# Performance work log

Measured on AMD Instinct MI355X. Metric: run time of the kernel, lower is better.

Reference implementation:

```python
import jax, jax.numpy as jnp
import numpy as np

FS = 2  # dilated kernel size
DILS = tuple(2 ** i for _ in range(2) for i in range(10))  # 2 blocks x 10 layers
LWS = tuple((FS - 1) * d for d in DILS)  # left-wing shrink of each dilated conv
TOTAL_LW = sum(LWS)  # 2046


def _conv(x, w, dil=1):
    # x: (B, Cin, T), w: (Cout, Cin, K), valid causal (left-wing) conv
    return jax.lax.conv_general_dilated(x, w, (1,), 'VALID', rhs_dilation=(dil,),
                                        dimension_numbers=('NCH', 'OIH', 'NCH'))


def _tconv(x, w, stride):
    # PyTorch ConvTranspose1d(n,n,k,stride,padding=k-stride): out_len = S*stride + stride - k
    wf = jnp.flip(w, -1).transpose(1, 0, 2)  # (in,out,k) -> (out,in,k), flipped taps
    return jax.lax.conv_general_dilated(x, wf, (1,), [(stride - 1, stride - 1)],
                                        lhs_dilation=(stride,),
                                        dimension_numbers=('NCH', 'OIH', 'NCH'))


def _wavenet(wav, lc_sparse, lc_conv_w, lc_conv_b, ups_w0, ups_b0, ups_w1, ups_b1,
             ups_w2, ups_b2, ups_w3, ups_b3, emb_w, emb_b, base_w, base_b,
             sig_w, sig_b, gate_w, gate_b, psig_w, pgate_w, skp_w, res_w,
             post1_w, post1_b, post2_w, post2_b, speaker_inds, jitter_index):
    # jitter local conditioning frames along time
    lc = jnp.take_along_axis(lc_sparse, jitter_index[:, None, :], axis=2)
    # post-jitter conv (kernel 3, valid)
    lc = _conv(lc, lc_conv_w) + lc_conv_b[:, None]
    # upsampling chain to audio rate
    for w, b, s in ((ups_w0, ups_b0, 5), (ups_w1, ups_b1, 4), (ups_w2, ups_b2, 4), (ups_w3, ups_b3, 4)):
        lc = _tconv(lc, w, s) + b[:, None]
    # global (speaker) conditioning: Linear applied to one-hot == column gather
    gc = emb_w[:, speaker_inds].T + emb_b  # (B, G)
    cond = jnp.concatenate(
        [lc, jnp.broadcast_to(gc[:, :, None], gc.shape + (lc.shape[2],))], axis=1)  # (B, I+G, T0)
    # base 1x1 conv onto residual channels; wav already trimmed to T0 = cond length
    x = _conv(wav, base_w) + base_b[:, None]
    skp_sum = jnp.zeros(())
    cum = 0
    for i, (dil, lw) in enumerate(zip(DILS, LWS)):
        cl = cum + lw                      # cond lead aligning cond to this layer's output
        c = cond[:, :, cl:]
        filt = _conv(x, sig_w[i], dil) + sig_b[i][:, None] + _conv(c, psig_w[i])
        gate = _conv(x, gate_w[i], dil) + gate_b[i][:, None] + _conv(c, pgate_w[i])
        z = jnp.tanh(filt) * jax.nn.sigmoid(gate)
        sl = TOTAL_LW - cl                 # skip lead aligning z to final output length
        skp_sum = skp_sum + _conv(z[:, :, sl:], skp_w[i])
        x = _conv(z, res_w[i]) + x[:, :, lw:]
        cum = cl
    h = jax.nn.relu(skp_sum)
    h = jax.nn.relu(_conv(h, post1_w) + post1_b[:, None])
    h = _conv(h, post2_w) + post2_b[:, None]
    return jax.nn.log_softmax(h, axis=1)  # (B, n_quant, T_final)


def setup_inputs() -> dict:
    key = jax.random.key(0)
    ks = iter(jax.random.split(key, 64))
    B, S = 4, 64
    NLC_IN, NLC_OUT, NSPK, NGE = 64, 128, 40, 128
    NQ, NR, ND, NS, NP = 256, 384, 256, 256, 512
    NCOND = NLC_OUT + NGE
    L = 20
    T = 18308  # (((64-2)*5+5-25)*4+4-16)... upsampled cond length == wav length

    def rn(shape, scale=0.05):
        return jax.random.normal(next(ks), shape, jnp.float32) * scale

    return dict(
        wav=rn((B, NQ, T), 1.0),
        lc_sparse=rn((B, NLC_IN, S), 1.0),
        lc_conv_w=rn((NLC_OUT, NLC_IN, 3)), lc_conv_b=rn((NLC_OUT,)),
        ups_w0=rn((NLC_OUT, NLC_OUT, 25)), ups_b0=rn((NLC_OUT,)),
        ups_w1=rn((NLC_OUT, NLC_OUT, 16)), ups_b1=rn((NLC_OUT,)),
        ups_w2=rn((NLC_OUT, NLC_OUT, 16)), ups_b2=rn((NLC_OUT,)),
        ups_w3=rn((NLC_OUT, NLC_OUT, 16)), ups_b3=rn((NLC_OUT,)),
        emb_w=rn((NGE, NSPK)), emb_b=rn((NGE,)),
        base_w=rn((NR, NQ, 1)), base_b=rn((NR,)),
        sig_w=rn((L, ND, NR, FS)), sig_b=rn((L, ND)),
        gate_w=rn((L, ND, NR, FS)), gate_b=rn((L, ND)),
        psig_w=rn((L, ND, NCOND, 1)), pgate_w=rn((L, ND, NCOND, 1)),
        skp_w=rn((L, NS, ND, 1)), res_w=rn((L, NR, ND, 1)),
        post1_w=rn((NP, NS, 1)), post1_b=rn((NP,)),
        post2_w=rn((NQ, NP, 1)), post2_b=rn((NQ,)),
        speaker_inds=jax.random.randint(next(ks), (B,), 0, NSPK),
        jitter_index=jax.random.randint(next(ks), (B, S), 0, S),
    )


def reference(wav, lc_sparse, lc_conv_w, lc_conv_b, ups_w0, ups_b0, ups_w1, ups_b1,
              ups_w2, ups_b2, ups_w3, ups_b3, emb_w, emb_b, base_w, base_b,
              sig_w, sig_b, gate_w, gate_b, psig_w, pgate_w, skp_w, res_w,
              post1_w, post1_b, post2_w, post2_b, speaker_inds, jitter_index):
    return _wavenet(wav, lc_sparse, lc_conv_w, lc_conv_b, ups_w0, ups_b0, ups_w1, ups_b1,
                    ups_w2, ups_b2, ups_w3, ups_b3, emb_w, emb_b, base_w, base_b,
                    sig_w, sig_b, gate_w, gate_b, psig_w, pgate_w, skp_w, res_w,
                    post1_w, post1_b, post2_w, post2_b, speaker_inds, jitter_index)
```

## Files before the change

kernel.cpp:

```cpp
#include <hip/hip_runtime.h>
#include <hip/hip_bf16.h>
#include <math.h>


#define T_IN 18308
#define T_OUT 16262

typedef unsigned short u16;
typedef unsigned int u32;
typedef __attribute__((ext_vector_type(8))) short short8_t;
typedef __attribute__((ext_vector_type(4))) float f32x4;

__device__ __forceinline__ float bf2f(u16 h) { return __uint_as_float(((u32)h) << 16); }
__device__ __forceinline__ u16 f2bf(float f) {
  u32 u = __float_as_uint(f);
  return (u16)((u + 0x7fffu + ((u >> 16) & 1u)) >> 16);
}

__global__ void k_pack_frag(const float* __restrict__ src, u16* __restrict__ dst,
                            int M, int K, int L, long src_lstride) {
  int nks = K >> 5;
  long per = (long)M * K;
  long total = per * L;
  for (long idx = blockIdx.x * (long)blockDim.x + threadIdx.x; idx < total; idx += (long)gridDim.x * blockDim.x) {
    int l = (int)(idx / per); long r = idx - (long)l * per;
    int j = (int)(r & 7); int lane = (int)((r >> 3) & 63); int fid = (int)(r >> 9);
    int ks = fid % nks; int mt = fid / nks;
    int row = mt * 16 + (lane & 15);
    int col = ks * 32 + ((lane >> 4) << 3) + j;
    dst[idx] = f2bf(src[l * src_lstride + (long)row * K + col]);
  }
}

__global__ void k_pack_frag_gau(const float* __restrict__ sig_w, const float* __restrict__ gate_w,
                                const float* __restrict__ psig_w, const float* __restrict__ pgate_w,
                                u16* __restrict__ dstF, u16* __restrict__ dstG) {
  const long per = 229376;
  long total = per * 20;
  for (long idx = blockIdx.x * (long)blockDim.x + threadIdx.x; idx < total; idx += (long)gridDim.x * blockDim.x) {
    int l = (int)(idx / per); long r = idx - (long)l * per;
    int j = (int)(r & 7); int lane = (int)((r >> 3) & 63); int fid = (int)(r >> 9);
    int ks = fid % 28; int mt = fid / 28;
    int row = mt * 16 + (lane & 15);
    int k = ks * 32 + ((lane >> 4) << 3) + j;
    float vF, vG;
    if (k < 384) {
      vF = sig_w[(((long)l * 256 + row) * 384 + k) * 2 + 0];
      vG = gate_w[(((long)l * 256 + row) * 384 + k) * 2 + 0];
    } else if (k < 768) {
      vF = sig_w[(((long)l * 256 + row) * 384 + (k - 384)) * 2 + 1];
      vG = gate_w[(((long)l * 256 + row) * 384 + (k - 384)) * 2 + 1];
    } else {
      vF = psig_w[((long)l * 256 + row) * 256 + (k - 768)];
      vG = pgate_w[((long)l * 256 + row) * 256 + (k - 768)];
    }
    dstF[idx] = f2bf(vF);
    dstG[idx] = f2bf(vG);
  }
}
// ... 123 lines not shown
    }
    __syncthreads();
  }
  #pragma unroll
  for (int jj = 0; jj < 4; ++jj) {
    int j = j0 + tn * 4 + jj;
    int t = j * S + p;
    if (t >= Lout) continue;
    #pragma unroll
    for (int i = 0; i < 4; ++i) {
      int o = bm0 + tm * 4 + i;
      yout[((long)b * 128 + o) * ostride + t] = acc[i][jj] + bias[o];
    }
  }
}

__global__ __launch_bounds__(256) void k_tconv4m(
    const u16* __restrict__ im, const u16* __restrict__ Wp4,
    const float* __restrict__ bias, u16* __restrict__ out) {
  int lane = threadIdx.x & 63, wave = threadIdx.x >> 6;
  int b = blockIdx.z;
  int p = blockIdx.y >> 1, chb = (blockIdx.y & 1) << 6;
  int tbase = (blockIdx.x << 8) + (wave << 6);
  int lrow = lane & 15, lk = (lane >> 4) << 3;
  int mt0 = chb >> 4;
  const u16* Wp = Wp4 + (long)p * 65536;
  f32x4 zed = {0.f, 0.f, 0.f, 0.f};
  f32x4 acc[4][4];
  #pragma unroll
  for (int m = 0; m < 4; ++m)
    #pragma unroll
    for (int n = 0; n < 4; ++n) acc[m][n] = zed;
  const u16* ib = im + (long)b * 4580 * 512;
  for (int ks = 0; ks < 16; ++ks) {
    short8_t a[4];
    #pragma unroll
    for (int m = 0; m < 4; ++m)
      a[m] = *(const short8_t*)(Wp + ((long)((mt0 + m) * 16 + ks) << 9) + (lane << 3));
    #pragma unroll
    for (int n = 0; n < 4; ++n) {
      int j = tbase + (n << 4) + lrow;
      j = min(j, 4579);
      short8_t bv = *(const short8_t*)(ib + (long)j * 512 + (ks << 5) + lk);
      #pragma unroll
      for (int m = 0; m < 4; ++m)
        acc[m][n] = __builtin_amdgcn_mfma_f32_16x16x32_bf16(a[m], bv, acc[m][n], 0, 0, 0);
    }
  }
  #pragma unroll
  for (int n = 0; n < 4; ++n) {
    int j = tbase + (n << 4) + lrow;
    int t = j * 4 + p;
    if (t >= T_IN) continue;
    #pragma unroll
    for (int m = 0; m < 4; ++m) {
      int ch0 = chb + (m << 4) + ((lane >> 4) << 2);
      f32x4 bb = *(const f32x4*)(bias + ch0);
      ushort4 o;
      o.x = f2bf(acc[m][n][0] + bb[0]);
      o.y = f2bf(acc[m][n][1] + bb[1]);
      o.z = f2bf(acc[m][n][2] + bb[2]);
      o.w = f2bf(acc[m][n][3] + bb[3]);
      *(ushort4*)(out + ((long)b * T_IN + t) * 128 + ch0) = o;
    }
  }
}

__global__ __launch_bounds__(256) void k_wav_t(const float* __restrict__ wav, u16* __restrict__ dst) {
  __shared__ float xs[32][65];
  int b = blockIdx.z, c0 = blockIdx.y * 32, t0 = blockIdx.x * 64;
  int tid = threadIdx.x;
  #pragma unroll
  for (int i = 0; i < 8; ++i) {
    int idx = tid + i * 256;
    int c = idx >> 6, tl = idx & 63;
    int t = t0 + tl; if (t >= T_IN) t = T_IN - 1;
    xs[c][tl] = wav[((long)b * 256 + c0 + c) * T_IN + t];
  }
  __syncthreads();
  #pragma unroll
  for (int i = 0; i < 8; ++i) {
    int idx = tid + i * 256;
    int tl = idx >> 5, c = idx & 31;
    int t = t0 + tl;
    if (t < T_IN) dst[((long)b * T_IN + t) * 256 + c0 + c] = f2bf(xs[c][tl]);
  }
}

__global__ __launch_bounds__(256) void k_basem(
    const u16* __restrict__ wavT, const u16* __restrict__ Wp,
    const float* __restrict__ bias, u16* __restrict__ X) {
  int lane = threadIdx.x & 63, wave = threadIdx.x >> 6;
  int b = blockIdx.z, chb = blockIdx.y << 6;
  int tbase = (blockIdx.x << 8) + (wave << 6);
  int lrow = lane & 15, lk = (lane >> 4) << 3;
  int mt0 = chb >> 4;
  f32x4 zed = {0.f, 0.f, 0.f, 0.f};
  f32x4 acc[4][4];
  #pragma unroll
  for (int m = 0; m < 4; ++m)
    #pragma unroll
    for (int n = 0; n < 4; ++n) acc[m][n] = zed;
  const u16* xb = wavT + (long)b * T_IN * 256;
  for (int ks = 0; ks < 8; ++ks) {
    short8_t a[4];
    #pragma unroll
    for (int m = 0; m < 4; ++m)
      a[m] = *(const short8_t*)(Wp + ((long)((mt0 + m) * 8 + ks) << 9) + (lane << 3));
    #pragma unroll
    for (int n = 0; n < 4; ++n) {
      int row = tbase + (n << 4) + lrow;
      row = min(row, T_IN - 1);
      short8_t bv = *(const short8_t*)(xb + (long)row * 256 + (ks << 5) + lk);
      #pragma unroll
      for (int m = 0; m < 4; ++m)
        acc[m][n] = __builtin_amdgcn_mfma_f32_16x16x32_bf16(a[m], bv, acc[m][n], 0, 0, 0);
    }
  }
  #pragma unroll
  for (int n = 0; n < 4; ++n) {
    int t = tbase + (n << 4) + lrow;
    if (t >= T_IN) continue;
    #pragma unroll
    for (int m = 0; m < 4; ++m) {
      int ch0 = chb + (m << 4) + ((lane >> 4) << 2);
      f32x4 bb = *(const f32x4*)(bias + ch0);
      ushort4 o;
      o.x = f2bf(acc[m][n][0] + bb[0]);
      o.y = f2bf(acc[m][n][1] + bb[1]);
      o.z = f2bf(acc[m][n][2] + bb[2]);
      o.w = f2bf(acc[m][n][3] + bb[3]);
      *(ushort4*)(X + ((long)b * T_IN + t) * 384 + ch0) = o;
    }
  }
}

__global__ __launch_bounds__(256, 3) void k_gau6(
    const u16* __restrict__ Xc, const u16* __restrict__ Lc,
    const u16* __restrict__ WpF, const u16* __restrict__ WpG,
    const float* __restrict__ cb, u16* __restrict__ Z,
    int Lz, int d, int cl, int nt) {
  __shared__ __align__(16) u16 stg[2][8192];
  int lane = threadIdx.x & 63, wave = threadIdx.x >> 6;
  int bx = blockIdx.x;
  int tb = ((bx >> 4) << 3) + (bx & 7);
  int chh = (bx >> 3) & 1;
  if (tb >= nt) return;
  int tbase = tb << 6;
  int b = blockIdx.z;
  int chb = (chh << 7) + (wave << 5);
  int mt0 = chb >> 4;
  int lrow = lane & 15, lk16 = lane >> 4;
  const u16* xb = Xc + (long)b * T_IN * 384;
  const u16* lb = Lc + (long)b * T_IN * 128;
  const u16* pWF0 = WpF + (((long)mt0 * 28) << 9) + (lane << 3);
  const u16* pWF1 = WpF + (((long)(mt0 + 1) * 28) << 9) + (lane << 3);
  const u16* pWG0 = WpG + (((long)mt0 * 28) << 9) + (lane << 3);
  const u16* pWG1 = WpG + (((long)(mt0 + 1) * 28) << 9) + (lane << 3);
  int r0 = tbase + (wave << 4) + lrow;
  const u16* s0 = xb + (long)min(r0, T_IN - 1) * 384 + (lk16 << 3);
  const u16* s1 = xb + (long)min(r0 + d, T_IN - 1) * 384 + (lk16 << 3);
  const u16* s2 = lb + (long)min(r0 + cl, T_IN - 1) * 128 + (lk16 << 3);
  u16* wd = &stg[0][0] + (wave << 9) + (lane << 3);

  f32x4 zed = {0.f, 0.f, 0.f, 0.f};
  f32x4 accF[2][4], accG[2][4];
  #pragma unroll
  for (int m = 0; m < 2; ++m)
    #pragma unroll
    for (int n = 0; n < 4; ++n) { accF[m][n] = zed; accG[m][n] = zed; }

  #pragma unroll
  for (int j = 0; j < 4; ++j)
    *(short8_t*)(wd + (j << 11)) = *(const short8_t*)(s0 + (j << 5));
  __syncthreads();

  #pragma unroll
  for (int ss = 0; ss < 7; ++ss) {
    short8_t nv0, nv1, nv2, nv3;
    if (ss < 6) {
      int kb = ss * 4 + 4;
      const u16* p0 = (kb + 0 < 12) ? (s0 + ((kb + 0) << 5)) : (kb + 0 < 24) ? (s1 + ((kb - 12) << 5)) : (s2 + ((kb - 24) << 5));
      const u16* p1 = (kb + 1 < 12) ? (s0 + ((kb + 1) << 5)) : (kb + 1 < 24) ? (s1 + ((kb - 11) << 5)) : (s2 + ((kb - 23) << 5));
      const u16* p2 = (kb + 2 < 12) ? (s0 + ((kb + 2) << 5)) : (kb + 2 < 24) ? (s1 + ((kb - 10) << 5)) : (s2 + ((kb - 22) << 5));
      const u16* p3 = (kb + 3 < 12) ? (s0 + ((kb + 3) << 5)) : (kb + 3 < 24) ? (s1 + ((kb - 9) << 5)) : (s2 + ((kb - 21) << 5));
      nv0 = *(const short8_t*)p0;
      nv1 = *(const short8_t*)p1;
      nv2 = *(const short8_t*)p2;
      nv3 = *(const short8_t*)p3;
    }
    const u16* bufc = &stg[ss & 1][0];
    #pragma unroll
    for (int j = 0; j < 4; ++j) {
      int ks = ss * 4 + j;
      short8_t af0 = *(const short8_t*)(pWF0 + (ks << 9));
      short8_t af1 = *(const short8_t*)(pWF1 + (ks << 9));
      short8_t ag0 = *(const short8_t*)(pWG0 + (ks << 9));
      short8_t ag1 = *(const short8_t*)(pWG1 + (ks << 9));
      #pragma unroll
      for (int n = 0; n < 4; ++n) {
        short8_t bv = *(const short8_t*)(bufc + (j << 11) + (n << 9) + (lane << 3));
        accF[0][n] = __builtin_amdgcn_mfma_f32_16x16x32_bf16(af0, bv, accF[0][n], 0, 0, 0);
        accF[1][n] = __builtin_amdgcn_mfma_f32_16x16x32_bf16(af1, bv, accF[1][n], 0, 0, 0);
        accG[0][n] = __builtin_amdgcn_mfma_f32_16x16x32_bf16(ag0, bv, accG[0][n], 0, 0, 0);
        accG[1][n] = __builtin_amdgcn_mfma_f32_16x16x32_bf16(ag1, bv, accG[1][n], 0, 0, 0);
      }
    }
    if (ss < 6) {
      u16* wdn = wd + (((ss + 1) & 1) << 13);
      *(short8_t*)(wdn + (0 << 11)) = nv0;
      *(short8_t*)(wdn + (1 << 11)) = nv1;
      *(short8_t*)(wdn + (2 << 11)) = nv2;
      *(short8_t*)(wdn + (3 << 11)) = nv3;
    }
    __syncthreads();
  }

  const float* cbF = cb + b * 256;
  const float* cbG = cb + 1024 + b * 256;
  #pragma unroll
  for (int n = 0; n < 4; ++n) {
    int t = tbase + (n << 4) + lrow;
    if (t >= Lz) continue;
    #pragma unroll
    for (int m = 0; m < 2; ++m) {
      int ch0 = chb + (m << 4) + (lk16 << 2);
      f32x4 bf = *(const f32x4*)(cbF + ch0);
      f32x4 bg = *(const f32x4*)(cbG + ch0);
      ushort4 o;
      #pragma unroll
      for (int r = 0; r < 4; ++r) {
        float f = accF[m][n][r] + bf[r];
        float g = accG[m][n][r] + bg[r];
        f = fminf(fmaxf(f, -15.f), 15.f);
        float e2 = __expf(2.f * f);
        float th = 1.f - 2.f * __builtin_amdgcn_rcpf(e2 + 1.f);
        float sg = __builtin_amdgcn_rcpf(1.f + __expf(-g));
        u16 zz = f2bf(th * sg);
        if (r == 0) o.x = zz; else if (r == 1) o.y = zz; else if (r == 2) o.z = zz; else o.w = zz;
      }
      *(ushort4*)(Z + ((long)b * T_IN + t) * 256 + ch0) = o;
    }
  }
}

__global__ __launch_bounds__(256, 3) void k_skipres6(
    const u16* __restrict__ Zb, const u16* __restrict__ Wskp, const u16* __restrict__ Wres,
    const u16* __restrict__ Xres, float* __restrict__ skip, u16* __restrict__ Xout,
    int Lz, int sl, int lw, int first) {
  __shared__ __align__(16) u16 stg[16384];
  int lane = threadIdx.x & 63, wave = threadIdx.x >> 6;
  int slice = blockIdx.x;
  int tbase = blockIdx.y << 6;
  int b = blockIdx.z;
  bool issk = slice < 2;
  int mt0 = (issk ? slice * 8 : (slice - 2) * 8) + (wave << 1);
  const u16* Wp = issk ? Wskp : Wres;
  int lrow = lane & 15, lk16 = lane >> 4;
  const u16* pW0 = Wp + (((long)mt0 * 8) << 9) + (lane << 3);
  const u16* pW1 = Wp + (((long)(mt0 + 1) * 8) << 9) + (lane << 3);
  const u16* zb = Zb + (long)b * T_IN * 256;
  int r0 = min(tbase + (wave << 4) + lrow, T_IN - 1);
  const u16* sz = zb + (long)r0 * 256 + (lk16 << 3);
  u16* wd = &stg[0] + (wave << 9) + (lane << 3);
  f32x4 zed = {0.f, 0.f, 0.f, 0.f};
  f32x4 acc[2][4];
  #pragma unroll
  for (int m = 0; m < 2; ++m)
    #pragma unroll
    for (int n = 0; n < 4; ++n) acc[m][n] = zed;

  #pragma unroll
  for (int j = 0; j < 8; ++j)
    *(short8_t*)(wd + (j << 11)) = *(const short8_t*)(sz + (j << 5));
  __syncthreads();

  #pragma unroll
  for (int ks = 0; ks < 8; ++ks) {
    short8_t a0 = *(const short8_t*)(pW0 + (ks << 9));
    short8_t a1 = *(const short8_t*)(pW1 + (ks << 9));
    #pragma unroll
    for (int n = 0; n < 4; ++n) {
      short8_t bv = *(const short8_t*)(&stg[0] + (ks << 11) + (n << 9) + (lane << 3));
      acc[0][n] = __builtin_amdgcn_mfma_f32_16x16x32_bf16(a0, bv, acc[0][n], 0, 0, 0);
      acc[1][n] = __builtin_amdgcn_mfma_f32_16x16x32_bf16(a1, bv, acc[1][n], 0, 0, 0);
    }
  }
  #pragma unroll
  for (int n = 0; n < 4; ++n) {
    int tg = tbase + (n << 4) + lrow;
    #pragma unroll
    for (int m = 0; m < 2; ++m) {
      int ch0 = ((mt0 + m) << 4) + (lk16 << 2);
      if (issk) {
        if (tg >= sl && tg < Lz) {
          float* p = skip + ((long)b * T_OUT + (tg - sl)) * 256 + ch0;
          if (first) { *(f32x4*)p = acc[m][n]; }
          else { f32x4 v = *(f32x4*)p; v += acc[m][n]; *(f32x4*)p = v; }
        }
      } else if (tg < Lz) {
        const u16* rp = Xres + ((long)b * T_IN + tg + lw) * 384 + ch0;
        ushort4 rv = *(const ushort4*)rp;
        ushort4 o;
        o.x = f2bf(acc[m][n][0] + bf2f(rv.x));
        o.y = f2bf(acc[m][n][1] + bf2f(rv.y));
        o.z = f2bf(acc[m][n][2] + bf2f(rv.z));
        o.w = f2bf(acc[m][n][3] + bf2f(rv.w));
        *(ushort4*)(Xout + ((long)b * T_IN + tg) * 384 + ch0) = o;
      }
    }
  }
}

__global__ __launch_bounds__(256) void k_post1(
    const float* __restrict__ skip, const u16* __restrict__ Wp,
    const float* __restrict__ b1, u16* __restrict__ h1) {
  int lane = threadIdx.x & 63, wave = threadIdx.x >> 6;
  int b = blockIdx.z, qb = blockIdx.y << 6;
  int tbase = (blockIdx.x << 8) + (wave << 6);
  int lrow = lane & 15, lk = (lane >> 4) << 3;
  int mt0 = qb >> 4;
  f32x4 zed = {0.f, 0.f, 0.f, 0.f};
  f32x4 acc[4][4];
  #pragma unroll
  for (int m = 0; m < 4; ++m)
    #pragma unroll
    for (int n = 0; n < 4; ++n) acc[m][n] = zed;
  const float* sb = skip + (long)b * T_OUT * 256;
  for (int ks = 0; ks < 8; ++ks) {
    short8_t a[4];
    #pragma unroll
    for (int m = 0; m < 4; ++m)
      a[m] = *(const short8_t*)(Wp + ((long)((mt0 + m) * 8 + ks) << 9) + (lane << 3));
    #pragma unroll
    for (int n = 0; n < 4; ++n) {
      int row = tbase + (n << 4) + lrow;
      row = min(row, T_OUT - 1);
      const float* src = sb + (long)row * 256 + (ks << 5) + lk;
      f32x4 v0 = *(const f32x4*)src;
      f32x4 v1 = *(const f32x4*)(src + 4);
      short8_t bv;
      #pragma unroll
      for (int j = 0; j < 4; ++j) bv[j] = (short)f2bf(fmaxf(v0[j], 0.f));
      #pragma unroll
      for (int j = 0; j < 4; ++j) bv[4 + j] = (short)f2bf(fmaxf(v1[j], 0.f));
      #pragma unroll
      for (int m = 0; m < 4; ++m)
        acc[m][n] = __builtin_amdgcn_mfma_f32_16x16x32_bf16(a[m], bv, acc[m][n], 0, 0, 0);
    }
  }
  #pragma unroll
  for (int n = 0; n < 4; ++n) {
    int t = tbase + (n << 4) + lrow;
    if (t >= T_OUT) continue;
    #pragma unroll
    for (int m = 0; m < 4; ++m) {
      int ch0 = qb + (m << 4) + ((lane >> 4) << 2);
      f32x4 bb = *(const f32x4*)(b1 + ch0);
      ushort4 o;
      o.x = f2bf(fmaxf(acc[m][n][0] + bb[0], 0.f));
      o.y = f2bf(fmaxf(acc[m][n][1] + bb[1], 0.f));
      o.z = f2bf(fmaxf(acc[m][n][2] + bb[2], 0.f));
      o.w = f2bf(fmaxf(acc[m][n][3] + bb[3], 0.f));
// ... 91 lines not shown
    }
  }
}

extern "C" void kernel_launch(void* const* d_in, const int* in_sizes, int n_in,
                              void* d_out, int out_size, void* d_ws, size_t ws_size,
                              hipStream_t stream) {
  const float* wav       = (const float*)d_in[0];
  const float* lc_sparse = (const float*)d_in[1];
  const float* lc_conv_w = (const float*)d_in[2];
  const float* lc_conv_b = (const float*)d_in[3];
  const float* ups_w[4]  = {(const float*)d_in[4], (const float*)d_in[6], (const float*)d_in[8], (const float*)d_in[10]};
  const float* ups_b[4]  = {(const float*)d_in[5], (const float*)d_in[7], (const float*)d_in[9], (const float*)d_in[11]};
  const float* emb_w     = (const float*)d_in[12];
  const float* emb_b     = (const float*)d_in[13];
  const float* base_w    = (const float*)d_in[14];
  const float* base_b    = (const float*)d_in[15];
  const float* sig_w     = (const float*)d_in[16];
  const float* sig_b     = (const float*)d_in[17];
  const float* gate_w    = (const float*)d_in[18];
  const float* gate_b    = (const float*)d_in[19];
  const float* psig_w    = (const float*)d_in[20];
  const float* pgate_w   = (const float*)d_in[21];
  const float* skp_w     = (const float*)d_in[22];
  const float* res_w     = (const float*)d_in[23];
  const float* post1_w   = (const float*)d_in[24];
  const float* post1_b   = (const float*)d_in[25];
  const float* post2_w   = (const float*)d_in[26];
  const float* post2_b   = (const float*)d_in[27];
  const int* spk         = (const int*)d_in[28];
  const int* jit         = (const int*)d_in[29];
  float* out = (float*)d_out;

  size_t off = 0;
  auto alloc = [&](size_t bytes) -> void* {
    off = (off + 255) & ~(size_t)255;
    void* p = (char*)d_ws + off;
    off += bytes;
    return p;
  };
  u16* wfgF   = (u16*)alloc(20L * 229376 * 2);
  u16* wfgG   = (u16*)alloc(20L * 229376 * 2);
  u16* wskpF  = (u16*)alloc(20L * 65536 * 2);
  u16* wresF  = (u16*)alloc(20L * 98304 * 2);
  u16* wbaseF = (u16*)alloc(384L * 256 * 2);
  u16* wp1F   = (u16*)alloc(512L * 256 * 2);
  u16* wp2F   = (u16*)alloc(256L * 512 * 2);
  float* wtc1 = (float*)alloc(5L * 640 * 128 * 4);
  float* wtc2 = (float*)alloc(4L * 512 * 128 * 4);
  float* wtc3 = (float*)alloc(4L * 512 * 128 * 4);
  u16* wtc4F  = (u16*)alloc(4L * 65536 * 2);
  float* cbias = (float*)alloc(20L * 2 * 4 * 256 * 4);
  float* gc    = (float*)alloc(4L * 128 * 4);
  u16* lcbf    = (u16*)alloc(4L * T_IN * 128 * 2);
  u16* xA      = (u16*)alloc(4L * T_IN * 384 * 2);
  u16* xB      = (u16*)alloc(4L * T_IN * 384 * 2);
  u16* zbuf    = (u16*)alloc(4L * T_IN * 256 * 2);
  float* skip  = (float*)alloc(4L * T_OUT * 256 * 4);
  float* lcs0 = (float*)zbuf;
  float* lcs1 = lcs0 + 4L * 128 * 64;
  float* lcs2 = lcs1 + 4L * 128 * 290;
  float* lcs3 = lcs2 + 4L * 128 * 1148;
  u16* im3    = xB;
  u16* wavT   = (u16*)skip;
  u16* h1bf   = xA;
  (void)ws_size; (void)in_sizes; (void)n_in; (void)out_size;

  k_pack_frag_gau<<<4480, 256, 0, stream>>>(sig_w, gate_w, psig_w, pgate_w, wfgF, wfgG);
  k_pack_frag<<<1280, 256, 0, stream>>>(skp_w, wskpF, 256, 256, 20, 256L * 256);
  k_pack_frag<<<1920, 256, 0, stream>>>(res_w, wresF, 384, 256, 20, 384L * 256);
  k_pack_frag<<<96, 256, 0, stream>>>(base_w, wbaseF, 384, 256, 1, 0);
  k_pack_frag<<<128, 256, 0, stream>>>(post1_w, wp1F, 512, 256, 1, 0);
  k_pack_frag<<<128, 256, 0, stream>>>(post2_w, wp2F, 256, 512, 1, 0);
  k_pack_tconv<<<320, 256, 0, stream>>>(ups_w[0], wtc1, 5, 25, 5);
  k_pack_tconv<<<256, 256, 0, stream>>>(ups_w[1], wtc2, 4, 16, 4);
  k_pack_tconv<<<256, 256, 0, stream>>>(ups_w[2], wtc3, 4, 16, 4);
  k_pack_tc4f<<<256, 256, 0, stream>>>(ups_w[3], wtc4F);
  k_gc<<<1, 512, 0, stream>>>(emb_w, emb_b, spk, gc);
  k_cbias<<<dim3(20, 8), 256, 0, stream>>>(psig_w, pgate_w, sig_b, gate_b, gc, cbias);

  k_lc0<<<dim3(4, 62), 128, 0, stream>>>(lc_sparse, jit, lc_conv_w, lc_conv_b, lcs0);
  k_tconvg<5><<<dim3(1, 10, 4), 256, 0, stream>>>(lcs0, 62, 64, lcs1, 290, 290, wtc1, ups_b[0], 5);
  k_tconvg<4><<<dim3(5, 8, 4), 256, 0, stream>>>(lcs1, 290, 290, lcs2, 1148, 1148, wtc2, ups_b[1], 4);
  k_tconvg<4><<<dim3(18, 8, 4), 256, 0, stream>>>(lcs2, 1148, 1148, lcs3, 4580, 4580, wtc3, ups_b[2], 4);
  k_im2col3<<<2048, 256, 0, stream>>>(lcs3, im3);
  k_tconv4m<<<dim3(18, 8, 4), 256, 0, stream>>>(im3, wtc4F, ups_b[3], lcbf);

  k_wav_t<<<dim3(287, 8, 4), 256, 0, stream>>>(wav, wavT);
  k_basem<<<dim3(72, 6, 4), 256, 0, stream>>>(wavT, wbaseF, base_b, xA);

  static const int DILS[20] = {1, 2, 4, 8, 16, 32, 64, 128, 256, 512,
                               1, 2, 4, 8, 16, 32, 64, 128, 256, 512};
  int cum = 0;
  u16* xc = xA; u16* xn = xB;
  for (int l = 0; l < 20; ++l) {
    int dd = DILS[l], lw = dd, cl = cum + lw;
    int Lz = T_IN - cl;
    int sl = 2046 - cl;
    int nt = (Lz + 63) / 64;
    int gx = 16 * ((nt + 7) >> 3);
    k_gau6<<<dim3(gx, 1, 4), 256, 0, stream>>>(
        xc, lcbf, wfgF + (long)l * 229376, wfgG + (long)l * 229376,
        cbias + (long)l * 2048, zbuf, Lz, dd, cl, nt);
    int nsl = (l == 19) ? 2 : 5;
    k_skipres6<<<dim3(nsl, nt, 4), 256, 0, stream>>>(
        zbuf, wskpF + (long)l * 65536, wresF + (long)l * 98304,
        xc, skip, xn, Lz, sl, lw, (l == 0) ? 1 : 0);
    cum = cl;
    u16* t = xc; xc = xn; xn = t;
  }

  k_post1<<<dim3(64, 8, 4), 256, 0, stream>>>(skip, wp1F, post1_b, h1bf);
  k_post2sm<<<dim3(255, 1, 4), 256, 0, stream>>>(h1bf, wp2F, post2_b, out);
}
```

Baseline: 3.617 ms.

## Store activations in MFMA fragment-tiled layout and load B operands directly

After: 4.530 ms. +25.2%, slower.

```diff
diff --git a/kernel.cpp b/kernel.cpp
--- a/kernel.cpp
+++ b/kernel.cpp
@@ -5,6 +5,10 @@
 
 #define T_IN 18308
 #define T_OUT 16262
+#define NT16 1152
+#define XTB (1152L * 12 * 512)
+#define ZTB (1152L * 8 * 512)
+#define LTB (1152L * 4 * 512)
 
 typedef unsigned short u16;
 typedef unsigned int u32;
@@ -234,6 +238,7 @@
     int j = tbase + (n << 4) + lrow;
     int t = j * 4 + p;
     if (t >= T_IN) continue;
+    int tt16 = t >> 4, tr = t & 15;
     #pragma unroll
     for (int m = 0; m < 4; ++m) {
       int ch0 = chb + (m << 4) + ((lane >> 4) << 2);
@@ -243,7 +248,8 @@
       o.y = f2bf(acc[m][n][1] + bb[1]);
       o.z = f2bf(acc[m][n][2] + bb[2]);
       o.w = f2bf(acc[m][n][3] + bb[3]);
-      *(ushort4*)(out + ((long)b * T_IN + t) * 128 + ch0) = o;
+      long addr = ((long)tt16 * 4 + (ch0 >> 5)) * 512 + ((ch0 & 31) >> 3) * 128 + tr * 8 + (ch0 & 7);
+      *(ushort4*)(out + (long)b * LTB + addr) = o;
     }
   }
 }
@@ -303,6 +309,7 @@
   for (int n = 0; n < 4; ++n) {
     int t = tbase + (n << 4) + lrow;
     if (t >= T_IN) continue;
+    int t16 = (tbase >> 4) + n;
     #pragma unroll
     for (int m = 0; m < 4; ++m) {
       int ch0 = chb + (m << 4) + ((lane >> 4) << 2);
@@ -312,39 +319,43 @@
       o.y = f2bf(acc[m][n][1] + bb[1]);
       o.z = f2bf(acc[m][n][2] + bb[2]);
       o.w = f2bf(acc[m][n][3] + bb[3]);
-      *(ushort4*)(X + ((long)b * T_IN + t) * 384 + ch0) = o;
-    }
-  }
-}
-
-__global__ __launch_bounds__(256, 3) void k_gau6(
+      long addr = ((long)t16 * 12 + (ch0 >> 5)) * 512 + ((ch0 & 31) >> 3) * 128 + lrow * 8 + (ch0 & 7);
+      *(ushort4*)(X + (long)b * XTB + addr) = o;
+    }
+  }
+}
+
+__global__ __launch_bounds__(256, 4) void k_gau7(
     const u16* __restrict__ Xc, const u16* __restrict__ Lc,
     const u16* __restrict__ WpF, const u16* __restrict__ WpG,
     const float* __restrict__ cb, u16* __restrict__ Z,
     int Lz, int d, int cl, int nt) {
-  __shared__ __align__(16) u16 stg[2][8192];
   int lane = threadIdx.x & 63, wave = threadIdx.x >> 6;
   int bx = blockIdx.x;
   int tb = ((bx >> 4) << 3) + (bx & 7);
   int chh = (bx >> 3) & 1;
   if (tb >= nt) return;
-  int tbase = tb << 6;
+  int tbase = tb << 6, tb4 = tb << 2;
   int b = blockIdx.z;
   int chb = (chh << 7) + (wave << 5);
   int mt0 = chb >> 4;
-  int lrow = lane & 15, lk16 = lane >> 4;
-  const u16* xb = Xc + (long)b * T_IN * 384;
-  const u16* lb = Lc + (long)b * T_IN * 128;
+  int lrow = lane & 15, loct = lane >> 4;
+  const u16* xb = Xc + (long)b * XTB;
+  const u16* lb = Lc + (long)b * LTB;
   const u16* pWF0 = WpF + (((long)mt0 * 28) << 9) + (lane << 3);
   const u16* pWF1 = WpF + (((long)(mt0 + 1) * 28) << 9) + (lane << 3);
   const u16* pWG0 = WpG + (((long)mt0 * 28) << 9) + (lane << 3);
   const u16* pWG1 = WpG + (((long)(mt0 + 1) * 28) << 9) + (lane << 3);
-  int r0 = tbase + (wave << 4) + lrow;
-  const u16* s0 = xb + (long)min(r0, T_IN - 1) * 384 + (lk16 << 3);
-  const u16* s1 = xb + (long)min(r0 + d, T_IN - 1) * 384 + (lk16 << 3);
-  const u16* s2 = lb + (long)min(r0 + cl, T_IN - 1) * 128 + (lk16 << 3);
-  u16* wd = &stg[0][0] + (wave << 9) + (lane << 3);
-
+  int P0[4], P1[4], P2[4];
+  #pragma unroll
+  for (int n = 0; n < 4; ++n) {
+    int T0 = tbase + (n << 4) + lrow;
+    P0[n] = (T0 >> 4) * 6144 + loct * 128 + (T0 & 15) * 8;
+    int T1 = T0 + d;
+    P1[n] = (T1 >> 4) * 6144 + loct * 128 + (T1 & 15) * 8;
+    int T2 = T0 + cl;
+    P2[n] = (T2 >> 4) * 2048 + loct * 128 + (T2 & 15) * 8;
+  }
   f32x4 zed = {0.f, 0.f, 0.f, 0.f};
   f32x4 accF[2][4], accG[2][4];
   #pragma unroll
@@ -353,49 +364,22 @@
     for (int n = 0; n < 4; ++n) { accF[m][n] = zed; accG[m][n] = zed; }
 
   #pragma unroll
-  for (int j = 0; j < 4; ++j)
-    *(short8_t*)(wd + (j << 11)) = *(const short8_t*)(s0 + (j << 5));
-  __syncthreads();
-
-  #pragma unroll
-  for (int ss = 0; ss < 7; ++ss) {
-    short8_t nv0, nv1, nv2, nv3;
-    if (ss < 6) {
-      int kb = ss * 4 + 4;
-      const u16* p0 = (kb + 0 < 12) ? (s0 + ((kb + 0) << 5)) : (kb + 0 < 24) ? (s1 + ((kb - 12) << 5)) : (s2 + ((kb - 24) << 5));
-      const u16* p1 = (kb + 1 < 12) ? (s0 + ((kb + 1) << 5)) : (kb + 1 < 24) ? (s1 + ((kb - 11) << 5)) : (s2 + ((kb - 23) << 5));
-      const u16* p2 = (kb + 2 < 12) ? (s0 + ((kb + 2) << 5)) : (kb + 2 < 24) ? (s1 + ((kb - 10) << 5)) : (s2 + ((kb - 22) << 5));
-      const u16* p3 = (kb + 3 < 12) ? (s0 + ((kb + 3) << 5)) : (kb + 3 < 24) ? (s1 + ((kb - 9) << 5)) : (s2 + ((kb - 21) << 5));
-      nv0 = *(const short8_t*)p0;
-      nv1 = *(const short8_t*)p1;
-      nv2 = *(const short8_t*)p2;
-      nv3 = *(const short8_t*)p3;
-    }
-    const u16* bufc = &stg[ss & 1][0];
-    #pragma unroll
-    for (int j = 0; j < 4; ++j) {
-      int ks = ss * 4 + j;
-      short8_t af0 = *(const short8_t*)(pWF0 + (ks << 9));
-      short8_t af1 = *(const short8_t*)(pWF1 + (ks << 9));
-      short8_t ag0 = *(const short8_t*)(pWG0 + (ks << 9));
-      short8_t ag1 = *(const short8_t*)(pWG1 + (ks << 9));
-      #pragma unroll
-      for (int n = 0; n < 4; ++n) {
-        short8_t bv = *(const short8_t*)(bufc + (j << 11) + (n << 9) + (lane << 3));
-        accF[0][n] = __builtin_amdgcn_mfma_f32_16x16x32_bf16(af0, bv, accF[0][n], 0, 0, 0);
-        accF[1][n] = __builtin_amdgcn_mfma_f32_16x16x32_bf16(af1, bv, accF[1][n], 0, 0, 0);
-        accG[0][n] = __builtin_amdgcn_mfma_f32_16x16x32_bf16(ag0, bv, accG[0][n], 0, 0, 0);
-        accG[1][n] = __builtin_amdgcn_mfma_f32_16x16x32_bf16(ag1, bv, accG[1][n], 0, 0, 0);
-      }
-    }
-    if (ss < 6) {
-      u16* wdn = wd + (((ss + 1) & 1) << 13);
-      *(short8_t*)(wdn + (0 << 11)) = nv0;
-      *(short8_t*)(wdn + (1 << 11)) = nv1;
-      *(short8_t*)(wdn + (2 << 11)) = nv2;
-      *(short8_t*)(wdn + (3 << 11)) = nv3;
-    }
-    __syncthreads();
+  for (int ks = 0; ks < 28; ++ks) {
+    short8_t af0 = *(const short8_t*)(pWF0 + (ks << 9));
+    short8_t af1 = *(const short8_t*)(pWF1 + (ks << 9));
+    short8_t ag0 = *(const short8_t*)(pWG0 + (ks << 9));
+    short8_t ag1 = *(const short8_t*)(pWG1 + (ks << 9));
+    #pragma unroll
+    for (int n = 0; n < 4; ++n) {
+      const u16* src = (ks < 12) ? (xb + P0[n] + (ks << 9))
+                     : (ks < 24) ? (xb + P1[n] + ((ks - 12) << 9))
+                                 : (lb + P2[n] + ((ks - 24) << 9));
+      short8_t bv = *(const short8_t*)src;
+      accF[0][n] = __builtin_amdgcn_mfma_f32_16x16x32_bf16(af0, bv, accF[0][n], 0, 0, 0);
+      accF[1][n] = __builtin_amdgcn_mfma_f32_16x16x32_bf16(af1, bv, accF[1][n], 0, 0, 0);
+      accG[0][n] = __builtin_amdgcn_mfma_f32_16x16x32_bf16(ag0, bv, accG[0][n], 0, 0, 0);
+      accG[1][n] = __builtin_amdgcn_mfma_f32_16x16x32_bf16(ag1, bv, accG[1][n], 0, 0, 0);
+    }
   }
 
   const float* cbF = cb + b * 256;
@@ -406,7 +390,7 @@
     if (t >= Lz) continue;
     #pragma unroll
     for (int m = 0; m < 2; ++m) {
-      int ch0 = chb + (m << 4) + (lk16 << 2);
+      int ch0 = chb + (m << 4) + (loct << 2);
       f32x4 bf = *(const f32x4*)(cbF + ch0);
       f32x4 bg = *(const f32x4*)(cbG + ch0);
       ushort4 o;
@@ -421,41 +405,36 @@
         u16 zz = f2bf(th * sg);
         if (r == 0) o.x = zz; else if (r == 1) o.y = zz; else if (r == 2) o.z = zz; else o.w = zz;
       }
-      *(ushort4*)(Z + ((long)b * T_IN + t) * 256 + ch0) = o;
-    }
-  }
-}
-
-__global__ __launch_bounds__(256, 3) void k_skipres6(
-    const u16* __restrict__ Zb, const u16* __restrict__ Wskp, const u16* __restrict__ Wres,
+      long addr = ((long)(tb4 + n) * 8 + (ch0 >> 5)) * 512 + ((ch0 & 31) >> 3) * 128 + lrow * 8 + (ch0 & 7);
+      *(ushort4*)(Z + (long)b * ZTB + addr) = o;
+    }
+  }
+}
+
+__global__ __launch_bounds__(256, 4) void k_skipres7(
+    const u16* __restrict__ Zt, const u16* __restrict__ Wskp, const u16* __restrict__ Wres,
     const u16* __restrict__ Xres, float* __restrict__ skip, u16* __restrict__ Xout,
     int Lz, int sl, int lw, int first) {
-  __shared__ __align__(16) u16 stg[16384];
   int lane = threadIdx.x & 63, wave = threadIdx.x >> 6;
   int slice = blockIdx.x;
-  int tbase = blockIdx.y << 6;
+  int tbase = blockIdx.y << 6, tb4 = blockIdx.y << 2;
   int b = blockIdx.z;
   bool issk = slice < 2;
   int mt0 = (issk ? slice * 8 : (slice - 2) * 8) + (wave << 1);
   const u16* Wp = issk ? Wskp : Wres;
-  int lrow = lane & 15, lk16 = lane >> 4;
+  int lrow = lane & 15, loct = lane >> 4;
   const u16* pW0 = Wp + (((long)mt0 * 8) << 9) + (lane << 3);
   const u16* pW1 = Wp + (((long)(mt0 + 1) * 8) << 9) + (lane << 3);
-  const u16* zb = Zb + (long)b * T_IN * 256;
-  int r0 = min(tbase + (wave << 4) + lrow, T_IN - 1);
-  const u16* sz = zb + (long)r0 * 256 + (lk16 << 3);
-  u16* wd = &stg[0] + (wave << 9) + (lane << 3);
+  const u16* zb = Zt + (long)b * ZTB;
+  int Pz[4];
+  #pragma unroll
+  for (int n = 0; n < 4; ++n) Pz[n] = ((tb4 + n) * 8) * 512 + lane * 8;
   f32x4 zed = {0.f, 0.f, 0.f, 0.f};
   f32x4 acc[2][4];
   #pragma unroll
   for (int m = 0; m < 2; ++m)
     #pragma unroll
     for (int n = 0; n < 4; ++n) acc[m][n] = zed;
-
-  #pragma unroll
-  for (int j = 0; j < 8; ++j)
-    *(short8_t*)(wd + (j << 11)) = *(const short8_t*)(sz + (j << 5));
-  __syncthreads();
 
   #pragma unroll
   for (int ks = 0; ks < 8; ++ks) {
@@ -463,7 +442,7 @@
     short8_t a1 = *(const short8_t*)(pW1 + (ks << 9));
     #pragma unroll
     for (int n = 0; n < 4; ++n) {
-      short8_t bv = *(const short8_t*)(&stg[0] + (ks << 11) + (n << 9) + (lane << 3));
+      short8_t bv = *(const short8_t*)(zb + Pz[n] + (ks << 9));
       acc[0][n] = __builtin_amdgcn_mfma_f32_16x16x32_bf16(a0, bv, acc[0][n], 0, 0, 0);
       acc[1][n] = __builtin_amdgcn_mfma_f32_16x16x32_bf16(a1, bv, acc[1][n], 0, 0, 0);
     }
@@ -473,7 +452,7 @@
     int tg = tbase + (n << 4) + lrow;
     #pragma unroll
     for (int m = 0; m < 2; ++m) {
-      int ch0 = ((mt0 + m) << 4) + (lk16 << 2);
+      int ch0 = ((mt0 + m) << 4) + (loct << 2);
       if (issk) {
         if (tg >= sl && tg < Lz) {
           float* p = skip + ((long)b * T_OUT + (tg - sl)) * 256 + ch0;
@@ -481,14 +460,16 @@
           else { f32x4 v = *(f32x4*)p; v += acc[m][n]; *(f32x4*)p = v; }
         }
       } else if (tg < Lz) {
-        const u16* rp = Xres + ((long)b * T_IN + tg + lw) * 384 + ch0;
-        ushort4 rv = *(const ushort4*)rp;
+        int T = tg + lw;
+        long ra = ((long)(T >> 4) * 12 + (ch0 >> 5)) * 512 + ((ch0 & 31) >> 3) * 128 + (T & 15) * 8 + (ch0 & 7);
+        ushort4 rv = *(const ushort4*)(Xres + (long)b * XTB + ra);
         ushort4 o;
         o.x = f2bf(acc[m][n][0] + bf2f(rv.x));
         o.y = f2bf(acc[m][n][1] + bf2f(rv.y));
         o.z = f2bf(acc[m][n][2] + bf2f(rv.z));
         o.w = f2bf(acc[m][n][3] + bf2f(rv.w));
-        *(ushort4*)(Xout + ((long)b * T_IN + tg) * 384 + ch0) = o;
+        long wa = ((long)(tb4 + n) * 12 + (ch0 >> 5)) * 512 + ((ch0 & 31) >> 3) * 128 + lrow * 8 + (ch0 & 7);
+        *(ushort4*)(Xout + (long)b * XTB + wa) = o;
       }
     }
   }
@@ -688,10 +669,10 @@
   u16* wtc4F  = (u16*)alloc(4L * 65536 * 2);
   float* cbias = (float*)alloc(20L * 2 * 4 * 256 * 4);
   float* gc    = (float*)alloc(4L * 128 * 4);
-  u16* lcbf    = (u16*)alloc(4L * T_IN * 128 * 2);
-  u16* xA      = (u16*)alloc(4L * T_IN * 384 * 2);
-  u16* xB      = (u16*)alloc(4L * T_IN * 384 * 2);
-  u16* zbuf    = (u16*)alloc(4L * T_IN * 256 * 2);
+  u16* lcbf    = (u16*)alloc(4L * LTB * 2);
+  u16* xA      = (u16*)alloc(4L * XTB * 2);
+  u16* xB      = (u16*)alloc(4L * XTB * 2);
+  u16* zbuf    = (u16*)alloc(4L * ZTB * 2);
   float* skip  = (float*)alloc(4L * T_OUT * 256 * 4);
   float* lcs0 = (float*)zbuf;
   float* lcs1 = lcs0 + 4L * 128 * 64;
@@ -735,11 +716,11 @@
     int sl = 2046 - cl;
     int nt = (Lz + 63) / 64;
     int gx = 16 * ((nt + 7) >> 3);
-    k_gau6<<<dim3(gx, 1, 4), 256, 0, stream>>>(
+    k_gau7<<<dim3(gx, 1, 4), 256, 0, stream>>>(
         xc, lcbf, wfgF + (long)l * 229376, wfgG + (long)l * 229376,
         cbias + (long)l * 2048, zbuf, Lz, dd, cl, nt);
     int nsl = (l == 19) ? 2 : 5;
-    k_skipres6<<<dim3(nsl, nt, 4), 256, 0, stream>>>(
+    k_skipres7<<<dim3(nsl, nt, 4), 256, 0, stream>>>(
         zbuf, wskpF + (long)l * 65536, wresF + (long)l * 98304,
         xc, skip, xn, Lz, sl, lw, (l == 0) ? 1 : 0);
     cum = cl;
```

## Split filter and gate GEMMs across waves with 128-step time tiles in gated unit

Applied to the files above, without the earlier changes.

Measured after the change: 3.686 ms. About the same (+1.9%).

```diff
diff --git a/kernel.cpp b/kernel.cpp
--- a/kernel.cpp
+++ b/kernel.cpp
@@ -317,28 +317,28 @@
   }
 }
 
-__global__ __launch_bounds__(256, 3) void k_gau6(
+__global__ __launch_bounds__(512, 4) void k_gau8(
     const u16* __restrict__ Xc, const u16* __restrict__ Lc,
     const u16* __restrict__ WpF, const u16* __restrict__ WpG,
     const float* __restrict__ cb, u16* __restrict__ Z,
     int Lz, int d, int cl, int nt) {
-  __shared__ __align__(16) u16 stg[2][8192];
+  __shared__ __align__(16) u16 stg[2][16384];
   int lane = threadIdx.x & 63, wave = threadIdx.x >> 6;
   int bx = blockIdx.x;
   int tb = ((bx >> 4) << 3) + (bx & 7);
   int chh = (bx >> 3) & 1;
   if (tb >= nt) return;
-  int tbase = tb << 6;
+  int tbase = tb << 7;
   int b = blockIdx.z;
-  int chb = (chh << 7) + (wave << 5);
+  int fg = wave & 1, chq = wave >> 1;
+  int chb = (chh << 7) + (chq << 5);
   int mt0 = chb >> 4;
   int lrow = lane & 15, lk16 = lane >> 4;
   const u16* xb = Xc + (long)b * T_IN * 384;
   const u16* lb = Lc + (long)b * T_IN * 128;
-  const u16* pWF0 = WpF + (((long)mt0 * 28) << 9) + (lane << 3);
-  const u16* pWF1 = WpF + (((long)(mt0 + 1) * 28) << 9) + (lane << 3);
-  const u16* pWG0 = WpG + (((long)mt0 * 28) << 9) + (lane << 3);
-  const u16* pWG1 = WpG + (((long)(mt0 + 1) * 28) << 9) + (lane << 3);
+  const u16* Wsel = fg ? WpG : WpF;
+  const u16* pW0 = Wsel + (((long)mt0 * 28) << 9) + (lane << 3);
+  const u16* pW1 = Wsel + (((long)(mt0 + 1) * 28) << 9) + (lane << 3);
   int r0 = tbase + (wave << 4) + lrow;
   const u16* s0 = xb + (long)min(r0, T_IN - 1) * 384 + (lk16 << 3);
   const u16* s1 = xb + (long)min(r0 + d, T_IN - 1) * 384 + (lk16 << 3);
@@ -346,18 +346,17 @@
   u16* wd = &stg[0][0] + (wave << 9) + (lane << 3);
 
   f32x4 zed = {0.f, 0.f, 0.f, 0.f};
-  f32x4 accF[2][4], accG[2][4];
+  f32x4 acc[2][8];
   #pragma unroll
   for (int m = 0; m < 2; ++m)
     #pragma unroll
-    for (int n = 0; n < 4; ++n) { accF[m][n] = zed; accG[m][n] = zed; }
+    for (int n = 0; n < 8; ++n) acc[m][n] = zed;
 
   #pragma unroll
   for (int j = 0; j < 4; ++j)
-    *(short8_t*)(wd + (j << 11)) = *(const short8_t*)(s0 + (j << 5));
+    *(short8_t*)(wd + (j << 12)) = *(const short8_t*)(s0 + (j << 5));
   __syncthreads();
 
-  #pragma unroll
   for (int ss = 0; ss < 7; ++ss) {
     short8_t nv0, nv1, nv2, nv3;
     if (ss < 6) {
@@ -375,53 +374,61 @@
     #pragma unroll
     for (int j = 0; j < 4; ++j) {
       int ks = ss * 4 + j;
-      short8_t af0 = *(const short8_t*)(pWF0 + (ks << 9));
-      short8_t af1 = *(const short8_t*)(pWF1 + (ks << 9));
-      short8_t ag0 = *(const short8_t*)(pWG0 + (ks << 9));
-      short8_t ag1 = *(const short8_t*)(pWG1 + (ks << 9));
-      #pragma unroll
-      for (int n = 0; n < 4; ++n) {
-        short8_t bv = *(const short8_t*)(bufc + (j << 11) + (n << 9) + (lane << 3));
-        accF[0][n] = __builtin_amdgcn_mfma_f32_16x16x32_bf16(af0, bv, accF[0][n], 0, 0, 0);
-        accF[1][n] = __builtin_amdgcn_mfma_f32_16x16x32_bf16(af1, bv, accF[1][n], 0, 0, 0);
-        accG[0][n] = __builtin_amdgcn_mfma_f32_16x16x32_bf16(ag0, bv, accG[0][n], 0, 0, 0);
-        accG[1][n] = __builtin_amdgcn_mfma_f32_16x16x32_bf16(ag1, bv, accG[1][n], 0, 0, 0);
+      short8_t a0 = *(const short8_t*)(pW0 + (ks << 9));
+      short8_t a1 = *(const short8_t*)(pW1 + (ks << 9));
+      #pragma unroll
+      for (int n = 0; n < 8; ++n) {
+        short8_t bv = *(const short8_t*)(bufc + (j << 12) + (n << 9) + (lane << 3));
+        acc[0][n] = __builtin_amdgcn_mfma_f32_16x16x32_bf16(a0, bv, acc[0][n], 0, 0, 0);
+        acc[1][n] = __builtin_amdgcn_mfma_f32_16x16x32_bf16(a1, bv, acc[1][n], 0, 0, 0);
       }
     }
     if (ss < 6) {
-      u16* wdn = wd + (((ss + 1) & 1) << 13);
-      *(short8_t*)(wdn + (0 << 11)) = nv0;
-      *(short8_t*)(wdn + (1 << 11)) = nv1;
-      *(short8_t*)(wdn + (2 << 11)) = nv2;
-      *(short8_t*)(wdn + (3 << 11)) = nv3;
+      u16* wdn = wd + (((ss + 1) & 1) << 14);
+      *(short8_t*)(wdn + (0 << 12)) = nv0;
+      *(short8_t*)(wdn + (1 << 12)) = nv1;
+      *(short8_t*)(wdn + (2 << 12)) = nv2;
+      *(short8_t*)(wdn + (3 << 12)) = nv3;
     }
     __syncthreads();
   }
 
-  const float* cbF = cb + b * 256;
-  const float* cbG = cb + 1024 + b * 256;
-  #pragma unroll
-  for (int n = 0; n < 4; ++n) {
-    int t = tbase + (n << 4) + lrow;
-    if (t >= Lz) continue;
-    #pragma unroll
-    for (int m = 0; m < 2; ++m) {
-      int ch0 = chb + (m << 4) + (lk16 << 2);
-      f32x4 bf = *(const f32x4*)(cbF + ch0);
-      f32x4 bg = *(const f32x4*)(cbG + ch0);
-      ushort4 o;
-      #pragma unroll
-      for (int r = 0; r < 4; ++r) {
-        float f = accF[m][n][r] + bf[r];
-        float g = accG[m][n][r] + bg[r];
-        f = fminf(fmaxf(f, -15.f), 15.f);
-        float e2 = __expf(2.f * f);
-        float th = 1.f - 2.f * __builtin_amdgcn_rcpf(e2 + 1.f);
-        float sg = __builtin_amdgcn_rcpf(1.f + __expf(-g));
-        u16 zz = f2bf(th * sg);
-        if (r == 0) o.x = zz; else if (r == 1) o.y = zz; else if (r == 2) o.z = zz; else o.w = zz;
+  float* xch = (float*)&stg[0][0];
+  if (fg == 0) {
+    #pragma unroll
+    for (int m = 0; m < 2; ++m)
+      #pragma unroll
+      for (int n = 0; n < 8; ++n)
+        *(f32x4*)&xch[(((((chq << 1) + m) << 3) + n) << 8) + (lane << 2)] = acc[m][n];
+  }
+  __syncthreads();
+  if (fg == 1) {
+    const float* cbF = cb + b * 256;
+    const float* cbG = cb + 1024 + b * 256;
+    #pragma unroll
+    for (int n = 0; n < 8; ++n) {
+      int t = tbase + (n << 4) + lrow;
+      if (t >= Lz) continue;
+      #pragma unroll
+      for (int m = 0; m < 2; ++m) {
+        int ch0 = chb + (m << 4) + (lk16 << 2);
+        f32x4 fv = *(const f32x4*)&xch[(((((chq << 1) + m) << 3) + n) << 8) + (lane << 2)];
+        f32x4 bf = *(const f32x4*)(cbF + ch0);
+        f32x4 bg = *(const f32x4*)(cbG + ch0);
+        ushort4 o;
+        #pragma unroll
+        for (int r = 0; r < 4; ++r) {
+          float f = fv[r] + bf[r];
+          float g = acc[m][n][r] + bg[r];
+          f = fminf(fmaxf(f, -15.f), 15.f);
+          float e2 = __expf(2.f * f);
+          float th = 1.f - 2.f * __builtin_amdgcn_rcpf(e2 + 1.f);
+          float sg = __builtin_amdgcn_rcpf(1.f + __expf(-g));
+          u16 zz = f2bf(th * sg);
+          if (r == 0) o.x = zz; else if (r == 1) o.y = zz; else if (r == 2) o.z = zz; else o.w = zz;
+        }
+        *(ushort4*)(Z + ((long)b * T_IN + t) * 256 + ch0) = o;
       }
-      *(ushort4*)(Z + ((long)b * T_IN + t) * 256 + ch0) = o;
     }
   }
 }
@@ -733,13 +740,14 @@
     int dd = DILS[l], lw = dd, cl = cum + lw;
     int Lz = T_IN - cl;
     int sl = 2046 - cl;
-    int nt = (Lz + 63) / 64;
-    int gx = 16 * ((nt + 7) >> 3);
-    k_gau6<<<dim3(gx, 1, 4), 256, 0, stream>>>(
+    int nt128 = (Lz + 127) / 128;
+    int gx = 16 * ((nt128 + 7) >> 3);
+    k_gau8<<<dim3(gx, 1, 4), 512, 0, stream>>>(
         xc, lcbf, wfgF + (long)l * 229376, wfgG + (long)l * 229376,
-        cbias + (long)l * 2048, zbuf, Lz, dd, cl, nt);
+        cbias + (long)l * 2048, zbuf, Lz, dd, cl, nt128);
+    int nt64 = (Lz + 63) / 64;
     int nsl = (l == 19) ? 2 : 5;
-    k_skipres6<<<dim3(nsl, nt, 4), 256, 0, stream>>>(
+    k_skipres6<<<dim3(nsl, nt64, 4), 256, 0, stream>>>(
         zbuf, wskpF + (long)l * 65536, wresF + (long)l * 98304,
         xc, skip, xn, Lz, sl, lw, (l == 0) ? 1 : 0);
     cum = cl;
```

## Keep skip/res weights in registers and loop four time tiles per block

Applied to the files above, without the earlier changes.

After: 3.825 ms. +5.8%, slower.

```diff
diff --git a/kernel.cpp b/kernel.cpp
--- a/kernel.cpp
+++ b/kernel.cpp
@@ -426,71 +426,93 @@
   }
 }
 
-__global__ __launch_bounds__(256, 3) void k_skipres6(
+__global__ __launch_bounds__(256, 3) void k_skipres8(
     const u16* __restrict__ Zb, const u16* __restrict__ Wskp, const u16* __restrict__ Wres,
     const u16* __restrict__ Xres, float* __restrict__ skip, u16* __restrict__ Xout,
     int Lz, int sl, int lw, int first) {
   __shared__ __align__(16) u16 stg[16384];
   int lane = threadIdx.x & 63, wave = threadIdx.x >> 6;
   int slice = blockIdx.x;
-  int tbase = blockIdx.y << 6;
+  int tb0 = blockIdx.y << 8;
   int b = blockIdx.z;
   bool issk = slice < 2;
   int mt0 = (issk ? slice * 8 : (slice - 2) * 8) + (wave << 1);
   const u16* Wp = issk ? Wskp : Wres;
   int lrow = lane & 15, lk16 = lane >> 4;
-  const u16* pW0 = Wp + (((long)mt0 * 8) << 9) + (lane << 3);
-  const u16* pW1 = Wp + (((long)(mt0 + 1) * 8) << 9) + (lane << 3);
+  short8_t w0[8], w1[8];
+  {
+    const u16* pW0 = Wp + (((long)mt0 * 8) << 9) + (lane << 3);
+    const u16* pW1 = Wp + (((long)(mt0 + 1) * 8) << 9) + (lane << 3);
+    #pragma unroll
+    for (int ks = 0; ks < 8; ++ks) {
+      w0[ks] = *(const short8_t*)(pW0 + (ks << 9));
+      w1[ks] = *(const short8_t*)(pW1 + (ks << 9));
+    }
+  }
   const u16* zb = Zb + (long)b * T_IN * 256;
-  int r0 = min(tbase + (wave << 4) + lrow, T_IN - 1);
-  const u16* sz = zb + (long)r0 * 256 + (lk16 << 3);
   u16* wd = &stg[0] + (wave << 9) + (lane << 3);
   f32x4 zed = {0.f, 0.f, 0.f, 0.f};
-  f32x4 acc[2][4];
-  #pragma unroll
-  for (int m = 0; m < 2; ++m)
-    #pragma unroll
-    for (int n = 0; n < 4; ++n) acc[m][n] = zed;
-
-  #pragma unroll
-  for (int j = 0; j < 8; ++j)
-    *(short8_t*)(wd + (j << 11)) = *(const short8_t*)(sz + (j << 5));
-  __syncthreads();
-
-  #pragma unroll
-  for (int ks = 0; ks < 8; ++ks) {
-    short8_t a0 = *(const short8_t*)(pW0 + (ks << 9));
-    short8_t a1 = *(const short8_t*)(pW1 + (ks << 9));
+
+  short8_t zr[8];
+  {
+    int r0 = min(tb0 + (wave << 4) + lrow, T_IN - 1);
+    const u16* sz = zb + (long)r0 * 256 + (lk16 << 3);
+    #pragma unroll
+    for (int j = 0; j < 8; ++j) zr[j] = *(const short8_t*)(sz + (j << 5));
+  }
+
+  for (int c = 0; c < 4; ++c) {
+    int tbase = tb0 + (c << 6);
+    if (tbase >= Lz) break;
+    #pragma unroll
+    for (int j = 0; j < 8; ++j) *(short8_t*)(wd + (j << 11)) = zr[j];
+    __syncthreads();
+    bool more = (c < 3) && (tb0 + ((c + 1) << 6) < Lz);
+    if (more) {
+      int r0 = min(tb0 + ((c + 1) << 6) + (wave << 4) + lrow, T_IN - 1);
+      const u16* sz = zb + (long)r0 * 256 + (lk16 << 3);
+      #pragma unroll
+      for (int j = 0; j < 8; ++j) zr[j] = *(const short8_t*)(sz + (j << 5));
+    }
+    f32x4 acc[2][4];
+    #pragma unroll
+    for (int m = 0; m < 2; ++m)
+      #pragma unroll
+      for (int n = 0; n < 4; ++n) acc[m][n] = zed;
+    #pragma unroll
+    for (int ks = 0; ks < 8; ++ks) {
+      #pragma unroll
+      for (int n = 0; n < 4; ++n) {
+        short8_t bv = *(const short8_t*)(&stg[0] + (ks << 11) + (n << 9) + (lane << 3));
+        acc[0][n] = __builtin_amdgcn_mfma_f32_16x16x32_bf16(w0[ks], bv, acc[0][n], 0, 0, 0);
+        acc[1][n] = __builtin_amdgcn_mfma_f32_16x16x32_bf16(w1[ks], bv, acc[1][n], 0, 0, 0);
+      }
+    }
     #pragma unroll
     for (int n = 0; n < 4; ++n) {
-      short8_t bv = *(const short8_t*)(&stg[0] + (ks << 11) + (n << 9) + (lane << 3));
-      acc[0][n] = __builtin_amdgcn_mfma_f32_16x16x32_bf16(a0, bv, acc[0][n], 0, 0, 0);
-      acc[1][n] = __builtin_amdgcn_mfma_f32_16x16x32_bf16(a1, bv, acc[1][n], 0, 0, 0);
-    }
-  }
-  #pragma unroll
-  for (int n = 0; n < 4; ++n) {
-    int tg = tbase + (n << 4) + lrow;
-    #pragma unroll
-    for (int m = 0; m < 2; ++m) {
-      int ch0 = ((mt0 + m) << 4) + (lk16 << 2);
-      if (issk) {
-        if (tg >= sl && tg < Lz) {
-          float* p = skip + ((long)b * T_OUT + (tg - sl)) * 256 + ch0;
-          if (first) { *(f32x4*)p = acc[m][n]; }
-          else { f32x4 v = *(f32x4*)p; v += acc[m][n]; *(f32x4*)p = v; }
+      int tg = tbase + (n << 4) + lrow;
+      #pragma unroll
+      for (int m = 0; m < 2; ++m) {
+        int ch0 = ((mt0 + m) << 4) + (lk16 << 2);
+        if (issk) {
+          if (tg >= sl && tg < Lz) {
+            float* p = skip + ((long)b * T_OUT + (tg - sl)) * 256 + ch0;
+            if (first) { *(f32x4*)p = acc[m][n]; }
+            else { f32x4 v = *(f32x4*)p; v += acc[m][n]; *(f32x4*)p = v; }
+          }
+        } else if (tg < Lz) {
+          const u16* rp = Xres + ((long)b * T_IN + tg + lw) * 384 + ch0;
+          ushort4 rv = *(const ushort4*)rp;
+          ushort4 o;
+          o.x = f2bf(acc[m][n][0] + bf2f(rv.x));
+          o.y = f2bf(acc[m][n][1] + bf2f(rv.y));
+          o.z = f2bf(acc[m][n][2] + bf2f(rv.z));
+          o.w = f2bf(acc[m][n][3] + bf2f(rv.w));
+          *(ushort4*)(Xout + ((long)b * T_IN + tg) * 384 + ch0) = o;
         }
-      } else if (tg < Lz) {
-        const u16* rp = Xres + ((long)b * T_IN + tg + lw) * 384 + ch0;
-        ushort4 rv = *(const ushort4*)rp;
-        ushort4 o;
-        o.x = f2bf(acc[m][n][0] + bf2f(rv.x));
-        o.y = f2bf(acc[m][n][1] + bf2f(rv.y));
-        o.z = f2bf(acc[m][n][2] + bf2f(rv.z));
-        o.w = f2bf(acc[m][n][3] + bf2f(rv.w));
-        *(ushort4*)(Xout + ((long)b * T_IN + tg) * 384 + ch0) = o;
       }
     }
+    if (more) __syncthreads();
   }
 }
 
@@ -738,8 +760,9 @@
     k_gau6<<<dim3(gx, 1, 4), 256, 0, stream>>>(
         xc, lcbf, wfgF + (long)l * 229376, wfgG + (long)l * 229376,
         cbias + (long)l * 2048, zbuf, Lz, dd, cl, nt);
+    int ntc = (Lz + 255) / 256;
     int nsl = (l == 19) ? 2 : 5;
-    k_skipres6<<<dim3(nsl, nt, 4), 256, 0, stream>>>(
+    k_skipres8<<<dim3(nsl, ntc, 4), 256, 0, stream>>>(
         zbuf, wskpF + (long)l * 65536, wresF + (long)l * 98304,
         xc, skip, xn, Lz, sl, lw, (l == 0) ? 1 : 0);
     cum = cl;
```
